# Performance work log

Hardware: AMD Instinct MI355X
Metric: run time of the kernel (lower is better)

Reference implementation:

```python
import jax, jax.numpy as jnp
import numpy as np

N_NODES = 100000
N_EDGES = 1600000
IN_DIM = 256
OUT_DIM = 128
EPS = 1e-12  # torch F.normalize default eps


def setup_inputs() -> dict:
    key = jax.random.key(0)
    k1, k2, k3, k4, k5 = jax.random.split(key, 5)
    x = jax.random.normal(k1, (N_NODES, IN_DIM), dtype=jnp.float32)
    edge_index = jax.random.randint(k2, (2, N_EDGES), 0, N_NODES, dtype=jnp.int64)
    # projection (no bias): weight [out, in]
    Wp = jax.random.normal(k3, (OUT_DIM, IN_DIM), dtype=jnp.float32) * 0.05
    # GCNConv internal linear weight [out, out] and output bias [out]
    Wg = jax.random.normal(k4, (OUT_DIM, OUT_DIM), dtype=jnp.float32) * 0.05
    bg = jax.random.normal(k5, (OUT_DIM,), dtype=jnp.float32) * 0.01
    return {"x": x, "edge_index": edge_index, "Wp": Wp, "Wg": Wg, "bg": bg}


def reference(x, edge_index, Wp, Wg, bg):
    n = x.shape[0]
    # projection: x @ Wp^T
    h = x @ Wp.T                      # [N, OUT]
    # GCNConv: transform first, then propagate
    h = h @ Wg.T                      # [N, OUT]
    # add self-loops
    loops = jnp.arange(n, dtype=edge_index.dtype)
    row = jnp.concatenate([edge_index[0], loops])   # source
    col = jnp.concatenate([edge_index[1], loops])   # target
    # symmetric normalization: deg over target index (edge_weight = 1)
    deg = jax.ops.segment_sum(jnp.ones_like(col, dtype=h.dtype), col, num_segments=n)
    dinv = jnp.where(deg > 0, jax.lax.rsqrt(deg), 0.0)
    norm = dinv[row] * dinv[col]                     # [E+N]
    # gather messages from source, scale, scatter-add to target
    msg = h[row] * norm[:, None]                     # [E+N, OUT]
    out = jax.ops.segment_sum(msg, col, num_segments=n)  # [N, OUT]
    out = out + bg
    # F.normalize(dim=1): divide by L2 norm clamped at eps
    nrm = jnp.sqrt(jnp.sum(out * out, axis=1, keepdims=True))
    out = out / jnp.maximum(nrm, EPS)
    return out
```

## Files before the change

### kernel.cpp

```cpp
#include <hip/hip_runtime.h>
#include <hip/hip_fp16.h>

#define NDIM 128
#define KDIM 256
#define MT 5
#define AROW 264
#define CHUNK 3200
#define BSH 9
#define BMASK 511
#define MAXBUCK 256
#define FTH 512
#define ECAP 12032
#define SFLAG 0x40000000

typedef _Float16 half8 __attribute__((ext_vector_type(8)));
typedef _Float16 half4v __attribute__((ext_vector_type(4)));
typedef _Float16 half2v __attribute__((ext_vector_type(2)));
typedef float float4v __attribute__((ext_vector_type(4)));

#if __has_builtin(__builtin_amdgcn_fdot2)
#define HAS_FDOT2 1
#else
#define HAS_FDOT2 0
#endif

__global__ __launch_bounds__(256) void k_prep(const float* __restrict__ Wp,
                                              const float* __restrict__ Wg,
                                              _Float16* __restrict__ Bfrag,
                                              const int* __restrict__ ei, int E,
                                              int* __restrict__ hist, int NBLK, int NBUCK,
                                              int* __restrict__ partials, int NSB) {
    __shared__ int h[MAXBUCK];
    int tid = threadIdx.x;
    int blk = blockIdx.x;
    if (blk < NBLK) {
        if (blk == 0 && tid < 128) {
            partials[tid] = 0;
        }
        const int* __restrict__ col = ei + E;
        h[tid] = 0;
        __syncthreads();
        int e0 = blk * CHUNK;
        int e1 = min(e0 + CHUNK, E);
        for (int e = e0 + tid; e < e1; e += 256) atomicAdd(&h[col[e] >> BSH], 1);
        __syncthreads();
        if (tid < NBUCK) hist[tid * NBLK + blk] = h[tid];
    } else {
        int o = blk - NBLK;
        int i = tid;
        float acc = 0.f;
#pragma unroll 4
        for (int k = 0; k < 128; ++k) acc = fmaf(Wg[o * 128 + k], Wp[k * 256 + i], acc);
        int kk = i >> 5, r = i & 31, quad = r >> 3, j = r & 7;
        int ntile = o >> 4, lanen = o & 15, lane = quad * 16 + lanen;
        Bfrag[(((ntile * 8 + kk) * 64) + lane) * 8 + j] = (_Float16)acc;
    }
}

__global__ __launch_bounds__(1024) void k_scan_lb(int* __restrict__ a, int n,
                                                  int* __restrict__ partials) {
    __shared__ int s[1024];
    int t = threadIdx.x;
    int blk = blockIdx.x;
    int i = blk * 1024 + t;
    int v = (i < n) ? a[i] : 0;
    s[t] = v;
    __syncthreads();
    for (int d = 1; d < 1024; d <<= 1) {
        int y = (t >= d) ? s[t - d] : 0;
        __syncthreads();
        s[t] += y;
        __syncthreads();
    }
    int myincl = s[t];
    int total = s[1023];
    if (t == 0)
        __hip_atomic_store(&partials[blk], total | SFLAG,
                           __ATOMIC_RELEASE, __HIP_MEMORY_SCOPE_AGENT);
    int contrib = 0;
    if (t < blk) {
        int pv;
        do {
            pv = __hip_atomic_load(&partials[t], __ATOMIC_ACQUIRE,
                                   __HIP_MEMORY_SCOPE_AGENT);
        } while (!(pv & SFLAG));
        contrib = pv & ~SFLAG;
    }
    __syncthreads();
    s[t] = contrib;
    __syncthreads();
    for (int d = 512; d > 0; d >>= 1) {
        if (t < d) s[t] += s[t + d];
        __syncthreads();
    }
    int excl = s[0];
    if (i < n) a[i] = myincl - v + excl;
}

__global__ __launch_bounds__(256) void k_phase3(const int* __restrict__ ei, int E,
                                                const int* __restrict__ offs, int NBLK, int NBUCK,
                                                int* __restrict__ tmp) {
    __shared__ int cur[MAXBUCK];
    int tid = threadIdx.x;
    if (tid < NBUCK) cur[tid] = offs[tid * NBLK + blockIdx.x];
    __syncthreads();
    int e0 = blockIdx.x * CHUNK;
    int e1 = min(e0 + CHUNK, E);
    for (int e = e0 + tid; e < e1; e += 256) {
        int r = ei[e];
        int c = ei[E + e];
        int p = atomicAdd(&cur[c >> BSH], 1);
        tmp[p] = (r << BSH) | (c & BMASK);
    }
}

__global__ __launch_bounds__(FTH, 1) void k_fine(const int* __restrict__ tmp,
                                                 const int* __restrict__ offs, int NBLK, int NBUCK,
                                                 int N, int E,
                                                 int* __restrict__ sortedRow,
                                                 int* __restrict__ cnt,
                                                 int* __restrict__ rowStart) {
    __shared__ int scnt[512];
    __shared__ int cur[512];
    __shared__ int ec[ECAP];
    int b = blockIdx.x;
    int t = threadIdx.x;
    int start = offs[b * NBLK];
    int end = (b + 1 < NBUCK) ? offs[(b + 1) * NBLK] : E;
    int len = end - start;

    scnt[t] = 0;
    __syncthreads();
    if (len <= ECAP) {
        for (int p = t; p < len; p += FTH) {
            int v = tmp[start + p];
            ec[p] = v;
            atomicAdd(&scnt[v & BMASK], 1);
        }
        __syncthreads();
        int v = scnt[t];
        for (int d = 1; d < 512; d <<= 1) {
            int y = (t >= d) ? scnt[t - d] : 0;
            __syncthreads();
            scnt[t] += y;
            __syncthreads();
        }
        int excl = scnt[t] - v;
        int node = (b << BSH) + t;
        if (node < N) {
            cnt[node] = v;
            rowStart[node] = start + excl;
        }
        cur[t] = start + excl;
        __syncthreads();
        for (int p = t; p < len; p += FTH) {
            int pr = ec[p];
            int slot = atomicAdd(&cur[pr & BMASK], 1);
            sortedRow[slot] = pr >> BSH;
        }
    } else {
        for (int p = start + t; p < end; p += FTH) atomicAdd(&scnt[tmp[p] & BMASK], 1);
        __syncthreads();
        int v = scnt[t];
        for (int d = 1; d < 512; d <<= 1) {
            int y = (t >= d) ? scnt[t - d] : 0;
            __syncthreads();
            scnt[t] += y;
            __syncthreads();
        }
        int excl = scnt[t] - v;
        int node = (b << BSH) + t;
        if (node < N) {
            cnt[node] = v;
            rowStart[node] = start + excl;
        }
        cur[t] = start + excl;
        __syncthreads();
        for (int p = start + t; p < end; p += FTH) {
            int pr = tmp[p];
            int slot = atomicAdd(&cur[pr & BMASK], 1);
            sortedRow[slot] = pr >> BSH;
        }
    }
    if (b == NBUCK - 1 && t == 0) rowStart[N] = E;
}

__global__ __launch_bounds__(256) void k_gemm_mfma(const float* __restrict__ x,
                                                   const _Float16* __restrict__ Bfrag,
                                                   const int* __restrict__ cnt,
                                                   _Float16* __restrict__ g, int nrows) {
    __shared__ __align__(16) _Float16 xs[2][16 * AROW];
    int tid  = threadIdx.x;
    int lane = tid & 63;
    int w    = tid >> 6;
    int quad = lane >> 4;
    int lcol = lane & 15;

    const half8* Bv = (const half8*)Bfrag;
    half8 b0[8], b1[8];
#pragma unroll
    for (int kk = 0; kk < 8; ++kk) {
        b0[kk] = Bv[(w * 8 + kk) * 64 + lane];
        b1[kk] = Bv[((w + 4) * 8 + kk) * 64 + lane];
    }

    long base = (long)blockIdx.x * (16 * MT);
    for (int t = 0; t < MT; ++t) {
        long m0 = base + t * 16;
        _Float16* xb = xs[t & 1];
        const float4* xv = (const float4*)(x + m0 * KDIM);
#pragma unroll
        for (int ii = 0; ii < 4; ++ii) {
            int idx = tid + ii * 256;
            int m = idx >> 6, k4 = idx & 63;
            float4 v = xv[idx];
            half4v hv = { (_Float16)v.x, (_Float16)v.y, (_Float16)v.z, (_Float16)v.w };
            *(half4v*)&xb[m * AROW + k4 * 4] = hv;
        }
        __syncthreads();

        float4v acc0 = {0.f, 0.f, 0.f, 0.f}, acc1 = {0.f, 0.f, 0.f, 0.f};
#pragma unroll
        for (int kk = 0; kk < 8; ++kk) {
            half8 a = *(const half8*)(&xb[lcol * AROW + kk * 32 + quad * 8]);
            acc0 = __builtin_amdgcn_mfma_f32_16x16x32_f16(a, b0[kk], acc0, 0, 0, 0);
            acc1 = __builtin_amdgcn_mfma_f32_16x16x32_f16(a, b1[kk], acc1, 0, 0, 0);
        }

#pragma unroll
        for (int r = 0; r < 4; ++r) {
            long node = m0 + quad * 4 + r;
            float di = rsqrtf((float)(cnt[node] + 1));
            g[node * NDIM + w * 16 + lcol]        = (_Float16)(acc0[r] * di);
            g[node * NDIM + (w + 4) * 16 + lcol]  = (_Float16)(acc1[r] * di);
        }
    }
}

__global__ __launch_bounds__(256) void k_gather(const _Float16* __restrict__ g,
                                                const int* __restrict__ rowStart,
                                                const int* __restrict__ sortedRow,
                                                const int* __restrict__ cnt,
                                                const float* __restrict__ bg,
                                                float* __restrict__ out) {
    int lane = threadIdx.x & 63;
    int i = blockIdx.x * 4 + (threadIdx.x >> 6);
    const int s = rowStart[i];
    const int e = rowStart[i + 1];
    const int g4  = lane >> 4;
    const int r16 = lane & 15;

    const half8* __restrict__ gv = (const half8*)g;

    float acc[8];
#pragma unroll
    for (int j = 0; j < 8; ++j) acc[j] = 0.f;

#if HAS_FDOT2
    const half2v one2 = { (_Float16)1.0f, (_Float16)1.0f };
#endif

    int p = s;
    for (; p + 16 <= e; p += 16) {
        int r0 = sortedRow[p + g4];
        int r1 = sortedRow[p + 4 + g4];
        int r2 = sortedRow[p + 8 + g4];
        int r3 = sortedRow[p + 12 + g4];
        half8 v0 = gv[(size_t)r0 * 16 + r16];
        half8 v1 = gv[(size_t)r1 * 16 + r16];
        half8 v2 = gv[(size_t)r2 * 16 + r16];
        half8 v3 = gv[(size_t)r3 * 16 + r16];
#if HAS_FDOT2
#pragma unroll
        for (int j = 0; j < 8; ++j) {
            half2v a = { v0[j], v1[j] };
            half2v b = { v2[j], v3[j] };
            acc[j] = __builtin_amdgcn_fdot2(a, one2,
                     __builtin_amdgcn_fdot2(b, one2, acc[j], false), false);
        }
#else
#pragma unroll
        for (int j = 0; j < 8; ++j)
            acc[j] += ((float)v0[j] + (float)v1[j]) + ((float)v2[j] + (float)v3[j]);
#endif
    }
    if (p + 8 <= e) {
        int r0 = sortedRow[p + g4];
        int r1 = sortedRow[p + 4 + g4];
        half8 v0 = gv[(size_t)r0 * 16 + r16];
        half8 v1 = gv[(size_t)r1 * 16 + r16];
#if HAS_FDOT2
#pragma unroll
        for (int j = 0; j < 8; ++j) {
            half2v a = { v0[j], v1[j] };
            acc[j] = __builtin_amdgcn_fdot2(a, one2, acc[j], false);
        }
#else
#pragma unroll
        for (int j = 0; j < 8; ++j) acc[j] += (float)v0[j] + (float)v1[j];
#endif
        p += 8;
    }
    if (p + 4 <= e) {
        int r0 = sortedRow[p + g4];
        half8 v0 = gv[(size_t)r0 * 16 + r16];
#pragma unroll
        for (int j = 0; j < 8; ++j) acc[j] += (float)v0[j];
        p += 4;
    }
    if (p + g4 < e) {
        int r0 = sortedRow[p + g4];
        half8 v0 = gv[(size_t)r0 * 16 + r16];
#pragma unroll
        for (int j = 0; j < 8; ++j) acc[j] += (float)v0[j];
    }

#pragma unroll
    for (int j = 0; j < 8; ++j) {
        acc[j] += __shfl_xor(acc[j], 16);
        acc[j] += __shfl_xor(acc[j], 32);
    }

    half8 sv = gv[(size_t)i * 16 + r16];
#pragma unroll
    for (int j = 0; j < 8; ++j) acc[j] += (float)sv[j];

    float di = rsqrtf((float)(cnt[i] + 1));
    float4 b0 = ((const float4*)bg)[r16 * 2];
    float4 b1 = ((const float4*)bg)[r16 * 2 + 1];
    float v[8];
    v[0] = fmaf(di, acc[0], b0.x);
    v[1] = fmaf(di, acc[1], b0.y);
    v[2] = fmaf(di, acc[2], b0.z);
    v[3] = fmaf(di, acc[3], b0.w);
    v[4] = fmaf(di, acc[4], b1.x);
    v[5] = fmaf(di, acc[5], b1.y);
    v[6] = fmaf(di, acc[6], b1.z);
    v[7] = fmaf(di, acc[7], b1.w);

    float sq = 0.f;
#pragma unroll
    for (int j = 0; j < 8; ++j) sq += v[j] * v[j];
    sq += __shfl_xor(sq, 1);
    sq += __shfl_xor(sq, 2);
    sq += __shfl_xor(sq, 4);
    sq += __shfl_xor(sq, 8);
    float scale = 1.0f / fmaxf(sqrtf(sq), 1e-12f);

    if (g4 == 0) {
        float4 o0 = make_float4(v[0] * scale, v[1] * scale, v[2] * scale, v[3] * scale);
        float4 o1 = make_float4(v[4] * scale, v[5] * scale, v[6] * scale, v[7] * scale);
        ((float4*)out)[(size_t)i * 32 + r16 * 2]     = o0;
        ((float4*)out)[(size_t)i * 32 + r16 * 2 + 1] = o1;
    }
}

extern "C" void kernel_launch(void* const* d_in, const int* in_sizes, int n_in,
                              void* d_out, int out_size, void* d_ws, size_t ws_size,
                              hipStream_t stream) {
    const float* x  = (const float*)d_in[0];
    const int*   ei = (const int*)  d_in[1];
    const float* Wp = (const float*)d_in[2];
    const float* Wg = (const float*)d_in[3];
    const float* bg = (const float*)d_in[4];
    float* out = (float*)d_out;

    const int N = in_sizes[0] / KDIM;
    const int E = in_sizes[1] / 2;

    const int NBLK  = (E + CHUNK - 1) / CHUNK;
    const int NBUCK = (N + BMASK) >> BSH;
    const int NE    = NBLK * NBUCK;
    const int NSB   = (NE + 1023) >> 10;

    char* p = (char*)d_ws;
    auto carve = [&](size_t bytes) { void* r = (void*)p; p += (bytes + 255) & ~(size_t)255; return r; };
    _Float16* g      = (_Float16*)carve((size_t)N * NDIM * 2);
    int*   sortedRow = (int*)  carve((size_t)E * 4);
    int*   tmp       = (int*)  carve((size_t)E * 4);
    _Float16* Bfrag  = (_Float16*)carve((size_t)KDIM * NDIM * 2);
    int*   cnt       = (int*)  carve((size_t)N * 4);
    int*   rowStart  = (int*)  carve((size_t)(N + 1) * 4);
    int*   hist      = (int*)  carve((size_t)NE * 4);
    int*   partials  = (int*)  carve((size_t)128 * 4);

    hipLaunchKernelGGL(k_prep, dim3(NBLK + 128), dim3(256), 0, stream,
                       Wp, Wg, Bfrag, ei, E, hist, NBLK, NBUCK, partials, NSB);
    hipLaunchKernelGGL(k_scan_lb, dim3(NSB), dim3(1024), 0, stream, hist, NE, partials);
    hipLaunchKernelGGL(k_phase3, dim3(NBLK), dim3(256), 0, stream, ei, E, hist, NBLK, NBUCK, tmp);
    hipLaunchKernelGGL(k_fine, dim3(NBUCK), dim3(FTH), 0, stream, tmp, hist, NBLK, NBUCK, N, E,
                       sortedRow, cnt, rowStart);
    hipLaunchKernelGGL(k_gemm_mfma, dim3(N / (16 * MT)), dim3(256), 0, stream, x, Bfrag, cnt, g, N);
    hipLaunchKernelGGL(k_gather, dim3(N / 4), dim3(256), 0, stream,
                       g, rowStart, sortedRow, cnt, bg, out);
}
```

Measured before the change: 296.6 us.

## Compute degrees with global atomics in histogram and co-launch fine sort with GEMM

Degree counts are now accumulated with global atomics during the bucket histogram pass, after a memset, instead of in the fine sort. The GEMM no longer depends on the fine sort, so both are merged into one launch where some blocks sort buckets and others run the MFMA projection, letting the small fine-sort grid overlap with GEMM work. Edge loads in the histogram and scatter passes are vectorized to int4. The cost is 1.6M global atomics on cnt, an extra memset, and 512-thread GEMM blocks with launch_bounds(512,1), which may limit occupancy.

```diff
diff --git a/kernel.cpp b/kernel.cpp
--- a/kernel.cpp
+++ b/kernel.cpp
@@ -12,6 +12,7 @@
 #define FTH 512
 #define ECAP 12032
 #define SFLAG 0x40000000
+#define SMEM_BYTES 52224
 
 typedef _Float16 half8 __attribute__((ext_vector_type(8)));
 typedef _Float16 half4v __attribute__((ext_vector_type(4)));
@@ -29,20 +30,32 @@
                                               _Float16* __restrict__ Bfrag,
                                               const int* __restrict__ ei, int E,
                                               int* __restrict__ hist, int NBLK, int NBUCK,
-                                              int* __restrict__ partials, int NSB) {
+                                              int* __restrict__ cnt,
+                                              int* __restrict__ partials) {
     __shared__ int h[MAXBUCK];
     int tid = threadIdx.x;
     int blk = blockIdx.x;
     if (blk < NBLK) {
-        if (blk == 0 && tid < 128) {
-            partials[tid] = 0;
-        }
+        if (blk == 0 && tid < 128) partials[tid] = 0;
         const int* __restrict__ col = ei + E;
         h[tid] = 0;
         __syncthreads();
         int e0 = blk * CHUNK;
         int e1 = min(e0 + CHUNK, E);
-        for (int e = e0 + tid; e < e1; e += 256) atomicAdd(&h[col[e] >> BSH], 1);
+        int lim = e1 - e0;
+        int lim4 = lim >> 2;
+        const int4* __restrict__ cv = (const int4*)(col + e0);
+        for (int q = tid; q < lim4; q += 256) {
+            int4 c = cv[q];
+            atomicAdd(&h[c.x >> BSH], 1); atomicAdd(&cnt[c.x], 1);
+            atomicAdd(&h[c.y >> BSH], 1); atomicAdd(&cnt[c.y], 1);
+            atomicAdd(&h[c.z >> BSH], 1); atomicAdd(&cnt[c.z], 1);
+            atomicAdd(&h[c.w >> BSH], 1); atomicAdd(&cnt[c.w], 1);
+        }
+        if (tid < (lim & 3)) {
+            int c = col[e0 + lim4 * 4 + tid];
+            atomicAdd(&h[c >> BSH], 1); atomicAdd(&cnt[c], 1);
+        }
         __syncthreads();
         if (tid < NBUCK) hist[tid * NBLK + blk] = h[tid];
     } else {
@@ -106,133 +119,147 @@
     __syncthreads();
     int e0 = blockIdx.x * CHUNK;
     int e1 = min(e0 + CHUNK, E);
-    for (int e = e0 + tid; e < e1; e += 256) {
-        int r = ei[e];
-        int c = ei[E + e];
+    int lim = e1 - e0;
+    int lim4 = lim >> 2;
+    const int4* __restrict__ rv4 = (const int4*)(ei + e0);
+    const int4* __restrict__ cv4 = (const int4*)(ei + E + e0);
+    for (int q = tid; q < lim4; q += 256) {
+        int4 r = rv4[q];
+        int4 c = cv4[q];
+        int p0 = atomicAdd(&cur[c.x >> BSH], 1); tmp[p0] = (r.x << BSH) | (c.x & BMASK);
+        int p1 = atomicAdd(&cur[c.y >> BSH], 1); tmp[p1] = (r.y << BSH) | (c.y & BMASK);
+        int p2 = atomicAdd(&cur[c.z >> BSH], 1); tmp[p2] = (r.z << BSH) | (c.z & BMASK);
+        int p3 = atomicAdd(&cur[c.w >> BSH], 1); tmp[p3] = (r.w << BSH) | (c.w & BMASK);
+    }
+    if (tid < (lim & 3)) {
+        int e = e0 + lim4 * 4 + tid;
+        int r = ei[e], c = ei[E + e];
         int p = atomicAdd(&cur[c >> BSH], 1);
         tmp[p] = (r << BSH) | (c & BMASK);
     }
 }
 
-__global__ __launch_bounds__(FTH, 1) void k_fine(const int* __restrict__ tmp,
-                                                 const int* __restrict__ offs, int NBLK, int NBUCK,
-                                                 int N, int E,
-                                                 int* __restrict__ sortedRow,
-                                                 int* __restrict__ cnt,
-                                                 int* __restrict__ rowStart) {
-    __shared__ int scnt[512];
-    __shared__ int cur[512];
-    __shared__ int ec[ECAP];
-    int b = blockIdx.x;
-    int t = threadIdx.x;
-    int start = offs[b * NBLK];
-    int end = (b + 1 < NBUCK) ? offs[(b + 1) * NBLK] : E;
-    int len = end - start;
-
-    scnt[t] = 0;
-    __syncthreads();
-    if (len <= ECAP) {
-        for (int p = t; p < len; p += FTH) {
-            int v = tmp[start + p];
-            ec[p] = v;
-            atomicAdd(&scnt[v & BMASK], 1);
-        }
-        __syncthreads();
-        int v = scnt[t];
-        for (int d = 1; d < 512; d <<= 1) {
-            int y = (t >= d) ? scnt[t - d] : 0;
+__global__ __launch_bounds__(FTH, 1) void k_fine_gemm(const int* __restrict__ tmp,
+                                                      const int* __restrict__ offs,
+                                                      int NBLK, int NBUCK,
+                                                      int N, int E,
+                                                      int* __restrict__ sortedRow,
+                                                      const int* __restrict__ cnt,
+                                                      int* __restrict__ rowStart,
+                                                      const float* __restrict__ x,
+                                                      const _Float16* __restrict__ Bfrag,
+                                                      _Float16* __restrict__ g) {
+    __shared__ __align__(16) char smem[SMEM_BYTES];
+    int tid = threadIdx.x;
+    int blk = blockIdx.x;
+
+    if (blk < NBUCK) {
+        int* scnt = (int*)smem;
+        int* cur  = scnt + 512;
+        int* ec   = cur + 512;
+        int b = blk;
+        int t = tid;
+        int start = offs[b * NBLK];
+        int end = (b + 1 < NBUCK) ? offs[(b + 1) * NBLK] : E;
+        int len = end - start;
+
+        scnt[t] = 0;
+        __syncthreads();
+        if (len <= ECAP) {
+            for (int p = t; p < len; p += FTH) {
+                int v = tmp[start + p];
+                ec[p] = v;
+                atomicAdd(&scnt[v & BMASK], 1);
+            }
             __syncthreads();
-            scnt[t] += y;
+            int v = scnt[t];
+            for (int d = 1; d < 512; d <<= 1) {
+                int y = (t >= d) ? scnt[t - d] : 0;
+                __syncthreads();
+                scnt[t] += y;
+                __syncthreads();
+            }
+            int excl = scnt[t] - v;
+            int node = (b << BSH) + t;
+            if (node < N) rowStart[node] = start + excl;
+            cur[t] = start + excl;
             __syncthreads();
-        }
-        int excl = scnt[t] - v;
-        int node = (b << BSH) + t;
-        if (node < N) {
-            cnt[node] = v;
-            rowStart[node] = start + excl;
-        }
-        cur[t] = start + excl;
-        __syncthreads();
-        for (int p = t; p < len; p += FTH) {
-            int pr = ec[p];
-            int slot = atomicAdd(&cur[pr & BMASK], 1);
-            sortedRow[slot] = pr >> BSH;
-        }
+            for (int p = t; p < len; p += FTH) {
+                int pr = ec[p];
+                int slot = atomicAdd(&cur[pr & BMASK], 1);
+                sortedRow[slot] = pr >> BSH;
+            }
+        } else {
+            for (int p = start + t; p < end; p += FTH) atomicAdd(&scnt[tmp[p] & BMASK], 1);
+            __syncthreads();
+            int v = scnt[t];
+            for (int d = 1; d < 512; d <<= 1) {
+                int y = (t >= d) ? scnt[t - d] : 0;
+                __syncthreads();
+                scnt[t] += y;
+                __syncthreads();
+            }
+            int excl = scnt[t] - v;
+            int node = (b << BSH) + t;
+            if (node < N) rowStart[node] = start + excl;
+            cur[t] = start + excl;
+            __syncthreads();
+            for (int p = start + t; p < end; p += FTH) {
+                int pr = tmp[p];
+                int slot = atomicAdd(&cur[pr & BMASK], 1);
+                sortedRow[slot] = pr >> BSH;
+            }
+        }
+        if (b == NBUCK - 1 && t == 0) rowStart[N] = E;
     } else {
-        for (int p = start + t; p < end; p += FTH) atomicAdd(&scnt[tmp[p] & BMASK], 1);
-        __syncthreads();
-        int v = scnt[t];
-        for (int d = 1; d < 512; d <<= 1) {
-            int y = (t >= d) ? scnt[t - d] : 0;
+        int bid = blk - NBUCK;
+        int t8   = tid & 255;
+        int sub  = tid >> 8;
+        int lane = t8 & 63;
+        int w    = t8 >> 6;
+        int quad = lane >> 4;
+        int lcol = lane & 15;
+
+        _Float16* xs = ((_Float16*)smem) + sub * (2 * 16 * AROW);
+
+        const half8* Bv = (const half8*)Bfrag;
+        half8 b0[8], b1[8];
+#pragma unroll
+        for (int kk = 0; kk < 8; ++kk) {
+            b0[kk] = Bv[(w * 8 + kk) * 64 + lane];
+            b1[kk] = Bv[((w + 4) * 8 + kk) * 64 + lane];
+        }
+
+        long base = (long)bid * (16 * MT * 2) + (long)sub * (16 * MT);
+        for (int t = 0; t < MT; ++t) {
+            long m0 = base + t * 16;
+            _Float16* xb = xs + (t & 1) * (16 * AROW);
+            const float4* xv = (const float4*)(x + m0 * KDIM);
+#pragma unroll
+            for (int ii = 0; ii < 4; ++ii) {
+                int idx = t8 + ii * 256;
+                int m = idx >> 6, k4 = idx & 63;
+                float4 v = xv[idx];
+                half4v hv = { (_Float16)v.x, (_Float16)v.y, (_Float16)v.z, (_Float16)v.w };
+                *(half4v*)&xb[m * AROW + k4 * 4] = hv;
+            }
             __syncthreads();
-            scnt[t] += y;
-            __syncthreads();
-        }
-        int excl = scnt[t] - v;
-        int node = (b << BSH) + t;
-        if (node < N) {
-            cnt[node] = v;
-            rowStart[node] = start + excl;
-        }
-        cur[t] = start + excl;
-        __syncthreads();
-        for (int p = start + t; p < end; p += FTH) {
-            int pr = tmp[p];
-            int slot = atomicAdd(&cur[pr & BMASK], 1);
-            sortedRow[slot] = pr >> BSH;
-        }
-    }
-    if (b == NBUCK - 1 && t == 0) rowStart[N] = E;
-}
-
-__global__ __launch_bounds__(256) void k_gemm_mfma(const float* __restrict__ x,
-                                                   const _Float16* __restrict__ Bfrag,
-                                                   const int* __restrict__ cnt,
-                                                   _Float16* __restrict__ g, int nrows) {
-    __shared__ __align__(16) _Float16 xs[2][16 * AROW];
-    int tid  = threadIdx.x;
-    int lane = tid & 63;
-    int w    = tid >> 6;
-    int quad = lane >> 4;
-    int lcol = lane & 15;
-
-    const half8* Bv = (const half8*)Bfrag;
-    half8 b0[8], b1[8];
-#pragma unroll
-    for (int kk = 0; kk < 8; ++kk) {
-        b0[kk] = Bv[(w * 8 + kk) * 64 + lane];
-        b1[kk] = Bv[((w + 4) * 8 + kk) * 64 + lane];
-    }
-
-    long base = (long)blockIdx.x * (16 * MT);
-    for (int t = 0; t < MT; ++t) {
-        long m0 = base + t * 16;
-        _Float16* xb = xs[t & 1];
-        const float4* xv = (const float4*)(x + m0 * KDIM);
-#pragma unroll
-        for (int ii = 0; ii < 4; ++ii) {
-            int idx = tid + ii * 256;
-            int m = idx >> 6, k4 = idx & 63;
-            float4 v = xv[idx];
-            half4v hv = { (_Float16)v.x, (_Float16)v.y, (_Float16)v.z, (_Float16)v.w };
-            *(half4v*)&xb[m * AROW + k4 * 4] = hv;
-        }
-        __syncthreads();
-
-        float4v acc0 = {0.f, 0.f, 0.f, 0.f}, acc1 = {0.f, 0.f, 0.f, 0.f};
-#pragma unroll
-        for (int kk = 0; kk < 8; ++kk) {
-            half8 a = *(const half8*)(&xb[lcol * AROW + kk * 32 + quad * 8]);
-            acc0 = __builtin_amdgcn_mfma_f32_16x16x32_f16(a, b0[kk], acc0, 0, 0, 0);
-            acc1 = __builtin_amdgcn_mfma_f32_16x16x32_f16(a, b1[kk], acc1, 0, 0, 0);
-        }
-
-#pragma unroll
-        for (int r = 0; r < 4; ++r) {
-            long node = m0 + quad * 4 + r;
-            float di = rsqrtf((float)(cnt[node] + 1));
-            g[node * NDIM + w * 16 + lcol]        = (_Float16)(acc0[r] * di);
-            g[node * NDIM + (w + 4) * 16 + lcol]  = (_Float16)(acc1[r] * di);
+
+            float4v acc0 = {0.f, 0.f, 0.f, 0.f}, acc1 = {0.f, 0.f, 0.f, 0.f};
+#pragma unroll
+            for (int kk = 0; kk < 8; ++kk) {
+                half8 a = *(const half8*)(&xb[lcol * AROW + kk * 32 + quad * 8]);
+                acc0 = __builtin_amdgcn_mfma_f32_16x16x32_f16(a, b0[kk], acc0, 0, 0, 0);
+                acc1 = __builtin_amdgcn_mfma_f32_16x16x32_f16(a, b1[kk], acc1, 0, 0, 0);
+            }
+
+#pragma unroll
+            for (int r = 0; r < 4; ++r) {
+                long node = m0 + quad * 4 + r;
+                float di = rsqrtf((float)(cnt[node] + 1));
+                g[node * NDIM + w * 16 + lcol]        = (_Float16)(acc0[r] * di);
+                g[node * NDIM + (w + 4) * 16 + lcol]  = (_Float16)(acc1[r] * di);
+            }
         }
     }
 }
@@ -372,6 +399,7 @@
     const int NBUCK = (N + BMASK) >> BSH;
     const int NE    = NBLK * NBUCK;
     const int NSB   = (NE + 1023) >> 10;
+    const int GBLK  = N / (16 * MT * 2);
 
     char* p = (char*)d_ws;
     auto carve = [&](size_t bytes) { void* r = (void*)p; p += (bytes + 255) & ~(size_t)255; return r; };
@@ -384,13 +412,13 @@
     int*   hist      = (int*)  carve((size_t)NE * 4);
     int*   partials  = (int*)  carve((size_t)128 * 4);
 
+    hipMemsetAsync(cnt, 0, (size_t)N * 4, stream);
     hipLaunchKernelGGL(k_prep, dim3(NBLK + 128), dim3(256), 0, stream,
-                       Wp, Wg, Bfrag, ei, E, hist, NBLK, NBUCK, partials, NSB);
+                       Wp, Wg, Bfrag, ei, E, hist, NBLK, NBUCK, cnt, partials);
     hipLaunchKernelGGL(k_scan_lb, dim3(NSB), dim3(1024), 0, stream, hist, NE, partials);
     hipLaunchKernelGGL(k_phase3, dim3(NBLK), dim3(256), 0, stream, ei, E, hist, NBLK, NBUCK, tmp);
-    hipLaunchKernelGGL(k_fine, dim3(NBUCK), dim3(FTH), 0, stream, tmp, hist, NBLK, NBUCK, N, E,
-                       sortedRow, cnt, rowStart);
-    hipLaunchKernelGGL(k_gemm_mfma, dim3(N / (16 * MT)), dim3(256), 0, stream, x, Bfrag, cnt, g, N);
+    hipLaunchKernelGGL(k_fine_gemm, dim3(NBUCK + GBLK), dim3(FTH), 0, stream,
+                       tmp, hist, NBLK, NBUCK, N, E, sortedRow, cnt, rowStart, x, Bfrag, g);
     hipLaunchKernelGGL(k_gather, dim3(N / 4), dim3(256), 0, stream,
                        g, rowStart, sortedRow, cnt, bg, out);
 }
```

Result: slower. 341.1 us (+15.0%).
